# Kernel tuning notes

Measured on AMD Instinct MI355X. Metric: run time of the kernel, lower is better.

## Reference

```python
import jax, jax.numpy as jnp
import numpy as np

N_NODES = 4096
N_EDGES = 262144
D = 128
N_REL = 1000
N_ENT = 50000


def setup_inputs() -> dict:
    key = jax.random.key(0)
    ks = jax.random.split(key, 6)
    x = jax.random.normal(ks[0], (N_NODES, D), dtype=jnp.float32)
    edge_index = jax.random.randint(ks[1], (2, N_EDGES), 0, N_NODES)
    relation_id = jax.random.randint(ks[2], (N_EDGES,), 0, N_REL)
    neg_flag = jax.random.randint(ks[3], (N_EDGES,), 0, 2)
    rel_emb = jax.random.normal(ks[4], (N_REL, D), dtype=jnp.float32)
    entity_emb = jax.random.normal(ks[5], (N_ENT, D), dtype=jnp.float32)
    scale = jnp.ones((N_ENT,), dtype=jnp.float32)
    bias = jnp.zeros((N_ENT,), dtype=jnp.float32)
    return {"x": x, "edge_index": edge_index, "relation_id": relation_id,
            "neg_flag": neg_flag, "rel_emb": rel_emb, "entity_emb": entity_emb,
            "scale": scale, "bias": bias}


def reference(x, edge_index, relation_id, neg_flag, rel_emb, entity_emb, scale, bias):
    src, dst = edge_index[0], edge_index[1]
    # message: gather x_j, TransE tail estimate, sign flip for negated atoms
    neg_coef = 1.0 - 2.0 * neg_flag.astype(x.dtype)           # [E]
    msg = (x[src] + rel_emb[relation_id]) * neg_coef[:, None]  # [E, D]
    # aggregate: scatter-add into target nodes
    aggr_out = jax.ops.segment_sum(msg, dst, num_segments=x.shape[0])  # [N, D]
    # update: residual + bias/scale double-matmul through entity table
    aggr = 0.1 * x + aggr_out                                  # [N, D]
    entity_score = aggr @ entity_emb.T                          # [N, V]
    entity_score = jax.nn.relu(entity_score * scale + bias)
    out = entity_score @ entity_emb                             # [N, D]
    return out
```

## Files before the change

kernel.cpp:

```cpp
#include <hip/hip_runtime.h>
#include <stdint.h>

typedef __attribute__((ext_vector_type(8))) short short8;
typedef __attribute__((ext_vector_type(8))) unsigned short ushort8;
typedef __attribute__((ext_vector_type(4))) float f32x4;
typedef __attribute__((ext_vector_type(16))) float f32x16;
typedef __attribute__((ext_vector_type(2))) unsigned int uint2v;

#define NNODES 4096
#define NEDGES 262144
#define DIM 128
#define NENT 50000
#define NENTP 50048
#define PREPB 782
#define ETILE 32
#define NT32 1563
#define NSPLIT 24

__device__ __forceinline__ unsigned short f2bf(float f) {
  union { __bf16 b; unsigned short u; } c;
  c.b = (__bf16)f;
  return c.u;
}

__global__ __launch_bounds__(1024) void k_scan(
    const int* __restrict__ cnt, int* __restrict__ off, int* __restrict__ cur)
{
  __shared__ int s[1024];
  int t = threadIdx.x;
  int4 v = reinterpret_cast<const int4*>(cnt)[t];
  int lsum = v.x + v.y + v.z + v.w;
  s[t] = lsum; __syncthreads();
  for (int d = 1; d < 1024; d <<= 1) {
    int a = (t >= d) ? s[t - d] : 0;
    __syncthreads();
    s[t] += a;
    __syncthreads();
  }
  int base = s[t] - lsum;
  int4 o; o.x = base; o.y = base + v.x; o.z = o.y + v.y; o.w = o.z + v.z;
  reinterpret_cast<int4*>(off)[t] = o;
  reinterpret_cast<int4*>(cur)[t] = o;
  if (t == 1023) off[4096] = base + lsum;
}

__global__ __launch_bounds__(256) void k_place(
    const int* __restrict__ ei, const int* __restrict__ rid,
    const int* __restrict__ nf, int* __restrict__ cur, int* __restrict__ sorted)
{
  int e = blockIdx.x * 256 + threadIdx.x;
  int dst = ei[NEDGES + e];
  int pos = atomicAdd(&cur[dst], 1);
  sorted[pos] = ei[e] | (rid[e] << 12) | (nf[e] << 22);
}

__global__ __launch_bounds__(256) void k_aggr(
    const int* __restrict__ off, const int* __restrict__ sorted,
    const float* __restrict__ x, const float* __restrict__ rel,
    unsigned short* __restrict__ q)
{
  __shared__ float sAcc[8 * 132];
  const int n = blockIdx.x;
  const int t = threadIdx.x;
  const int slot = t >> 5;
  const int c = t & 31;
  const int b = off[n], eN = off[n + 1];
  float4 acc = make_float4(0.f, 0.f, 0.f, 0.f);
  for (int i = b + slot; i < eN; i += 8) {
    int p = sorted[i];
    float4 xv = reinterpret_cast<const float4*>(x)[(p & 4095) * 32 + c];
    float4 rv = reinterpret_cast<const float4*>(rel)[((p >> 12) & 1023) * 32 + c];
    float sgn = (p & (1 << 22)) ? -1.f : 1.f;
    acc.x += sgn * (xv.x + rv.x);
    acc.y += sgn * (xv.y + rv.y);
    acc.z += sgn * (xv.z + rv.z);
    acc.w += sgn * (xv.w + rv.w);
  }
  *reinterpret_cast<float4*>(&sAcc[slot * 132 + c * 4]) = acc;
  __syncthreads();
  if (t < 128) {
    float s = 0.f;
#pragma unroll
    for (int k = 0; k < 8; ++k) s += sAcc[k * 132 + t];
    q[n * DIM + t] = f2bf(0.1f * x[n * DIM + t] + s);
  }
}

__global__ __launch_bounds__(256) void k_prep(
    const float* __restrict__ ent, const float* __restrict__ scale,
    unsigned short* __restrict__ ebf, unsigned short* __restrict__ etbf,
    const int* __restrict__ ei, int* __restrict__ cnt)
{
  if (blockIdx.x >= PREPB) {
    int e = (blockIdx.x - PREPB) * 256 + threadIdx.x;
    atomicAdd(&cnt[ei[NEDGES + e]], 1);
    return;
  }
  __shared__ float sT[64 * 133];
  const int t = threadIdx.x;
  const int e0 = blockIdx.x * 64;
#pragma unroll
  for (int i = 0; i < 8; ++i) {
    int idx = i * 256 + t;
    int e = idx >> 5;
    int c4 = idx & 31;
    float4 v = make_float4(0.f, 0.f, 0.f, 0.f);
    float sc = 0.f;
    if (e0 + e < NENT) {
      v = reinterpret_cast<const float4*>(ent)[(e0 + e) * 32 + c4];
      sc = scale[e0 + e];
    }
    *reinterpret_cast<float4*>(&sT[e * 133 + c4 * 4]) = v;
    ushort4 bq;
    bq.x = f2bf(v.x * sc); bq.y = f2bf(v.y * sc);
    bq.z = f2bf(v.z * sc); bq.w = f2bf(v.w * sc);
    *reinterpret_cast<ushort4*>(&ebf[(e0 + e) * 128 + c4 * 4]) = bq;
  }
  __syncthreads();
  const int lane = t & 63;
  const int w = t >> 6;
  const int dl = lane >> 3;
  const int el = (lane & 7) * 8;
#pragma unroll
  for (int it = 0; it < 4; ++it) {
    int d = it * 32 + w * 8 + dl;
    ushort8 buf;
#pragma unroll
    for (int j = 0; j < 8; ++j) buf[j] = f2bf(sT[(el + j) * 133 + d]);
    *reinterpret_cast<ushort8*>(&etbf[d * NENTP + e0 + el]) = buf;
  }
}


__device__ __forceinline__ void gll16(const void* g, void* l) {
  __builtin_amdgcn_global_load_lds(
      (const __attribute__((address_space(1))) unsigned int*)g,
      (__attribute__((address_space(3))) unsigned int*)l, 16, 0, 0);
}

__device__ __forceinline__ unsigned cvtpk(float lo, float hi) {
  unsigned r;
  asm("v_cvt_pk_bf16_f32 %0, %1, %2" : "=v"(r) : "v"(lo), "v"(hi));
  return r;
}

__global__ __launch_bounds__(256, 3) void k_flash(
    const unsigned short* __restrict__ qg,
    const unsigned short* __restrict__ ebf,
    const unsigned short* __restrict__ etbf,
    const float* __restrict__ bias,
    float* __restrict__ out)
{
  __shared__ __align__(16) unsigned short sE[2][ETILE * 128];
  __shared__ __align__(16) unsigned short sET[2][128 * ETILE];
  __shared__ __align__(16) float sBias[2][ETILE];

  const int t = threadIdx.x;
  const int w = t >> 6;
  const int lane = t & 63;
  const int l31 = lane & 31;
  const int hi = lane >> 5;

  const int m0 = blockIdx.x * 128;
  const int tile_lo = (blockIdx.y * NT32) / NSPLIT;
  const int tile_hi = ((blockIdx.y + 1) * NT32) / NSPLIT;

  const int cE = (((t & 15) ^ ((t >> 4) & 15))) * 8;
  const int rE = t >> 4;
  const int cT = (((t & 3) ^ ((t >> 4) & 3))) * 8;
  const int rT = t >> 2;

  short8 qf[8];
  {
    const unsigned short* qrow = qg + (size_t)(m0 + w * 32 + l31) * DIM + hi * 8;
#pragma unroll
    for (int kk = 0; kk < 8; ++kk)
      qf[kk] = *reinterpret_cast<const short8*>(qrow + kk * 16);
  }

  f32x16 accO[4];
#pragma unroll
  for (int td = 0; td < 4; ++td)
#pragma unroll
    for (int r = 0; r < 16; ++r) accO[td][r] = 0.f;

  {
    const int vt = tile_lo * ETILE;
#pragma unroll
    for (int i = 0; i < 2; ++i)
      gll16(ebf + (size_t)(vt + i * 16 + rE) * DIM + cE, &sE[0][(i * 256 + t) * 8]);
#pragma unroll
    for (int i = 0; i < 2; ++i)
      gll16(etbf + (size_t)(i * 64 + rT) * NENTP + vt + cT, &sET[0][(i * 256 + t) * 8]);
    if (t < ETILE) sBias[0][t] = (vt + t < NENT) ? bias[vt + t] : 0.f;
  }
  __syncthreads();

  int cur = 0;
  for (int tile = tile_lo; tile < tile_hi; ++tile) {
    if (tile + 1 < tile_hi) {
      const int vt = (tile + 1) * ETILE;
#pragma unroll
      for (int i = 0; i < 2; ++i)
        gll16(ebf + (size_t)(vt + i * 16 + rE) * DIM + cE,
              &sE[cur ^ 1][(i * 256 + t) * 8]);
#pragma unroll
      for (int i = 0; i < 2; ++i)
        gll16(etbf + (size_t)(i * 64 + rT) * NENTP + vt + cT,
              &sET[cur ^ 1][(i * 256 + t) * 8]);
      if (t < ETILE) sBias[cur ^ 1][t] = (vt + t < NENT) ? bias[vt + t] : 0.f;
    }

    const unsigned short* sEc = sE[cur];
    const float* sb = sBias[cur];
    f32x16 accA, accB;
#pragma unroll
    for (int r = 0; r < 16; ++r) { accA[r] = 0.f; accB[r] = 0.f; }

    __builtin_amdgcn_s_setprio(1);
#pragma unroll
    for (int kk = 0; kk < 4; ++kk) {
      const int colA = ((kk * 4 + hi) ^ (l31 & 15)) * 8;
      const int colB = ((kk * 4 + 2 + hi) ^ (l31 & 15)) * 8;
      short8 a0 = *reinterpret_cast<const short8*>(&sEc[l31 * 128 + colA]);
      short8 a1 = *reinterpret_cast<const short8*>(&sEc[l31 * 128 + colB]);
      accA = __builtin_amdgcn_mfma_f32_32x32x16_bf16(a0, qf[2 * kk], accA, 0, 0, 0);
      accB = __builtin_amdgcn_mfma_f32_32x32x16_bf16(a1, qf[2 * kk + 1], accB, 0, 0, 0);
    }
    __builtin_amdgcn_s_setprio(0);

    short8 F[2];
    {
      float p[16];
#pragma unroll
      for (int g = 0; g < 4; ++g) {
        f32x4 b4 = *reinterpret_cast<const f32x4*>(&sb[g * 8 + hi * 4]);
#pragma unroll
        for (int j = 0; j < 4; ++j)
          p[g * 4 + j] = fmaxf(accA[g * 4 + j] + accB[g * 4 + j] + b4[j], 0.f);
      }
      unsigned wr[8];
#pragma unroll
      for (int c2 = 0; c2 < 8; ++c2) wr[c2] = cvtpk(p[2 * c2], p[2 * c2 + 1]);
      uint2v r02 = __builtin_amdgcn_permlane32_swap(wr[0], wr[2], false, false);
      uint2v r13 = __builtin_amdgcn_permlane32_swap(wr[1], wr[3], false, false);
      uint2v r46 = __builtin_amdgcn_permlane32_swap(wr[4], wr[6], false, false);
      uint2v r57 = __builtin_amdgcn_permlane32_swap(wr[5], wr[7], false, false);
      union { unsigned u[4]; short8 s; } f0, f1;
      f0.u[0] = r02[0]; f0.u[1] = r13[0]; f0.u[2] = r02[1]; f0.u[3] = r13[1];
      f1.u[0] = r46[0]; f1.u[1] = r57[0]; f1.u[2] = r46[1]; f1.u[3] = r57[1];
      F[0] = f0.s;
      F[1] = f1.s;
    }

    const unsigned short* sTc = sET[cur];
    const int keyT = (l31 >> 2) & 3;
    __builtin_amdgcn_s_setprio(1);
#pragma unroll
    for (int ke = 0; ke < 2; ++ke) {
      const int col = ((ke * 2 + hi) ^ keyT) * 8;
#pragma unroll
      for (int td = 0; td < 4; ++td) {
        const int d = td * 32 + l31;
        short8 bT = *reinterpret_cast<const short8*>(&sTc[d * ETILE + col]);
        accO[td] = __builtin_amdgcn_mfma_f32_32x32x16_bf16(F[ke], bT, accO[td], 0, 0, 0);
      }
    }
    __builtin_amdgcn_s_setprio(0);

    __syncthreads();
    cur ^= 1;
  }

#pragma unroll
  for (int td = 0; td < 4; ++td) {
#pragma unroll
    for (int r = 0; r < 16; ++r) {
      int qrow = (r & 3) + 8 * (r >> 2) + 4 * hi;
      int row = m0 + w * 32 + qrow;
      int col = td * 32 + l31;
      atomicAdd(&out[(size_t)row * DIM + col], accO[td][r]);
    }
  }
}

extern "C" void kernel_launch(void* const* d_in, const int* in_sizes, int n_in,
                              void* d_out, int out_size, void* d_ws, size_t ws_size,
                              hipStream_t stream) {
  const float* x     = (const float*)d_in[0];
  const int*   ei    = (const int*)d_in[1];
  const int*   rid   = (const int*)d_in[2];
  const int*   nf    = (const int*)d_in[3];
  const float* rel   = (const float*)d_in[4];
  const float* ent   = (const float*)d_in[5];
  const float* scale = (const float*)d_in[6];
  const float* bias  = (const float*)d_in[7];
  float* out = (float*)d_out;

  char* ws = (char*)d_ws;
  int*            cnt    = (int*)(ws + 0);
  int*            off    = (int*)(ws + (16u << 10));
  int*            cur    = (int*)(ws + (36u << 10));
  int*            sorted = (int*)(ws + (64u << 10));
  unsigned short* qb     = (unsigned short*)(ws + (1344u << 10));
  unsigned short* ebf    = (unsigned short*)(ws + (2560u << 10));
  unsigned short* etbf   = (unsigned short*)(ws + (2560u << 10) + (size_t)NENTP * DIM * 2);

  hipMemsetAsync(cnt, 0, 4096 * sizeof(int), stream);
  hipMemsetAsync(d_out, 0, (size_t)out_size * sizeof(float), stream);
  k_prep<<<PREPB + NEDGES / 256, 256, 0, stream>>>(ent, scale, ebf, etbf, ei, cnt);
  k_scan<<<1, 1024, 0, stream>>>(cnt, off, cur);
  k_place<<<NEDGES / 256, 256, 0, stream>>>(ei, rid, nf, cur, sorted);
  k_aggr<<<NNODES, 256, 0, stream>>>(off, sorted, x, rel, qb);
  k_flash<<<dim3(NNODES / 128, NSPLIT), 256, 0, stream>>>(qb, ebf, etbf, bias, out);
}
```

Baseline: 270.0 us.

## Software-pipeline score and output GEMMs with triple-buffered LDS tiles

Moves the entity-tile loop to a triple-buffered software pipeline. The score MFMAs for tile i+1 are issued alongside the output MFMAs for tile i, and loads run two tiles ahead. The aim is to hide the dependency stall between the score GEMM, the bias/ReLU/bf16 repack and the output GEMM, and to give global loads more lead time. LDS use per block grows by half, which could cut occupancy under the 3-blocks-per-CU launch bound.

```diff
diff --git a/kernel.cpp b/kernel.cpp
--- a/kernel.cpp
+++ b/kernel.cpp
@@ -151,9 +151,9 @@
     const float* __restrict__ bias,
     float* __restrict__ out)
 {
-  __shared__ __align__(16) unsigned short sE[2][ETILE * 128];
-  __shared__ __align__(16) unsigned short sET[2][128 * ETILE];
-  __shared__ __align__(16) float sBias[2][ETILE];
+  __shared__ __align__(16) unsigned short sE[3][ETILE * 128];
+  __shared__ __align__(16) unsigned short sET[3][128 * ETILE];
+  __shared__ __align__(16) float sBias[3][ETILE];
 
   const int t = threadIdx.x;
   const int w = t >> 6;
@@ -184,40 +184,22 @@
 #pragma unroll
     for (int r = 0; r < 16; ++r) accO[td][r] = 0.f;
 
-  {
-    const int vt = tile_lo * ETILE;
-#pragma unroll
-    for (int i = 0; i < 2; ++i)
-      gll16(ebf + (size_t)(vt + i * 16 + rE) * DIM + cE, &sE[0][(i * 256 + t) * 8]);
-#pragma unroll
-    for (int i = 0; i < 2; ++i)
-      gll16(etbf + (size_t)(i * 64 + rT) * NENTP + vt + cT, &sET[0][(i * 256 + t) * 8]);
-    if (t < ETILE) sBias[0][t] = (vt + t < NENT) ? bias[vt + t] : 0.f;
-  }
-  __syncthreads();
-
-  int cur = 0;
-  for (int tile = tile_lo; tile < tile_hi; ++tile) {
-    if (tile + 1 < tile_hi) {
-      const int vt = (tile + 1) * ETILE;
-#pragma unroll
-      for (int i = 0; i < 2; ++i)
-        gll16(ebf + (size_t)(vt + i * 16 + rE) * DIM + cE,
-              &sE[cur ^ 1][(i * 256 + t) * 8]);
-#pragma unroll
-      for (int i = 0; i < 2; ++i)
-        gll16(etbf + (size_t)(i * 64 + rT) * NENTP + vt + cT,
-              &sET[cur ^ 1][(i * 256 + t) * 8]);
-      if (t < ETILE) sBias[cur ^ 1][t] = (vt + t < NENT) ? bias[vt + t] : 0.f;
-    }
-
-    const unsigned short* sEc = sE[cur];
-    const float* sb = sBias[cur];
-    f32x16 accA, accB;
+  f32x16 accA, accB;
+  short8 F[2];
+
+  auto STAGE = [&](int tile, int buf) {
+    const int vt = tile * ETILE;
+    gll16(ebf + (size_t)(vt + rE) * DIM + cE, &sE[buf][t * 8]);
+    gll16(ebf + (size_t)(vt + 16 + rE) * DIM + cE, &sE[buf][(256 + t) * 8]);
+    gll16(etbf + (size_t)rT * NENTP + vt + cT, &sET[buf][t * 8]);
+    gll16(etbf + (size_t)(64 + rT) * NENTP + vt + cT, &sET[buf][(256 + t) * 8]);
+    if (t < ETILE) sBias[buf][t] = (vt + t < NENT) ? bias[vt + t] : 0.f;
+  };
+
+  auto SPHASE = [&](int buf) {
+    const unsigned short* sEc = sE[buf];
 #pragma unroll
     for (int r = 0; r < 16; ++r) { accA[r] = 0.f; accB[r] = 0.f; }
-
-    __builtin_amdgcn_s_setprio(1);
 #pragma unroll
     for (int kk = 0; kk < 4; ++kk) {
       const int colA = ((kk * 4 + hi) ^ (l31 & 15)) * 8;
@@ -227,35 +209,35 @@
       accA = __builtin_amdgcn_mfma_f32_32x32x16_bf16(a0, qf[2 * kk], accA, 0, 0, 0);
       accB = __builtin_amdgcn_mfma_f32_32x32x16_bf16(a1, qf[2 * kk + 1], accB, 0, 0, 0);
     }
-    __builtin_amdgcn_s_setprio(0);
-
-    short8 F[2];
-    {
-      float p[16];
-#pragma unroll
-      for (int g = 0; g < 4; ++g) {
-        f32x4 b4 = *reinterpret_cast<const f32x4*>(&sb[g * 8 + hi * 4]);
-#pragma unroll
-        for (int j = 0; j < 4; ++j)
-          p[g * 4 + j] = fmaxf(accA[g * 4 + j] + accB[g * 4 + j] + b4[j], 0.f);
-      }
-      unsigned wr[8];
-#pragma unroll
-      for (int c2 = 0; c2 < 8; ++c2) wr[c2] = cvtpk(p[2 * c2], p[2 * c2 + 1]);
-      uint2v r02 = __builtin_amdgcn_permlane32_swap(wr[0], wr[2], false, false);
-      uint2v r13 = __builtin_amdgcn_permlane32_swap(wr[1], wr[3], false, false);
-      uint2v r46 = __builtin_amdgcn_permlane32_swap(wr[4], wr[6], false, false);
-      uint2v r57 = __builtin_amdgcn_permlane32_swap(wr[5], wr[7], false, false);
-      union { unsigned u[4]; short8 s; } f0, f1;
-      f0.u[0] = r02[0]; f0.u[1] = r13[0]; f0.u[2] = r02[1]; f0.u[3] = r13[1];
-      f1.u[0] = r46[0]; f1.u[1] = r57[0]; f1.u[2] = r46[1]; f1.u[3] = r57[1];
-      F[0] = f0.s;
-      F[1] = f1.s;
-    }
-
-    const unsigned short* sTc = sET[cur];
+  };
+
+  auto REPACK = [&](int buf) {
+    const float* sb = sBias[buf];
+    float p[16];
+#pragma unroll
+    for (int g = 0; g < 4; ++g) {
+      f32x4 b4 = *reinterpret_cast<const f32x4*>(&sb[g * 8 + hi * 4]);
+#pragma unroll
+      for (int j = 0; j < 4; ++j)
+        p[g * 4 + j] = fmaxf(accA[g * 4 + j] + accB[g * 4 + j] + b4[j], 0.f);
+    }
+    unsigned wr[8];
+#pragma unroll
+    for (int c2 = 0; c2 < 8; ++c2) wr[c2] = cvtpk(p[2 * c2], p[2 * c2 + 1]);
+    uint2v r02 = __builtin_amdgcn_permlane32_swap(wr[0], wr[2], false, false);
+    uint2v r13 = __builtin_amdgcn_permlane32_swap(wr[1], wr[3], false, false);
+    uint2v r46 = __builtin_amdgcn_permlane32_swap(wr[4], wr[6], false, false);
+    uint2v r57 = __builtin_amdgcn_permlane32_swap(wr[5], wr[7], false, false);
+    union { unsigned u[4]; short8 s; } f0, f1;
+    f0.u[0] = r02[0]; f0.u[1] = r13[0]; f0.u[2] = r02[1]; f0.u[3] = r13[1];
+    f1.u[0] = r46[0]; f1.u[1] = r57[0]; f1.u[2] = r46[1]; f1.u[3] = r57[1];
+    F[0] = f0.s;
+    F[1] = f1.s;
+  };
+
+  auto OPHASE = [&](int buf) {
+    const unsigned short* sTc = sET[buf];
     const int keyT = (l31 >> 2) & 3;
-    __builtin_amdgcn_s_setprio(1);
 #pragma unroll
     for (int ke = 0; ke < 2; ++ke) {
       const int col = ((ke * 2 + hi) ^ keyT) * 8;
@@ -266,11 +248,31 @@
         accO[td] = __builtin_amdgcn_mfma_f32_32x32x16_bf16(F[ke], bT, accO[td], 0, 0, 0);
       }
     }
+  };
+
+  STAGE(tile_lo, 0);
+  if (tile_lo + 1 < tile_hi) STAGE(tile_lo + 1, 1);
+  __syncthreads();
+  SPHASE(0);
+
+  int cur = 0;
+  for (int tile = tile_lo; tile < tile_hi - 1; ++tile) {
+    int nx = cur + 1; if (nx == 3) nx = 0;
+    int st = nx + 1; if (st == 3) st = 0;
+    if (tile + 2 < tile_hi) STAGE(tile + 2, st);
+    REPACK(cur);
+    __builtin_amdgcn_s_setprio(1);
+    SPHASE(nx);
+    OPHASE(cur);
     __builtin_amdgcn_s_setprio(0);
-
     __syncthreads();
-    cur ^= 1;
-  }
+    cur = nx;
+  }
+
+  REPACK(cur);
+  __builtin_amdgcn_s_setprio(1);
+  OPHASE(cur);
+  __builtin_amdgcn_s_setprio(0);
 
 #pragma unroll
   for (int td = 0; td < 4; ++td) {
```

Measured after the change: 276.2 us. 2.3% more time.

## Fuse prep, scan, place and aggregate into one cooperative persistent kernel

Applied to the files above, without the earlier changes.

Merges the four preprocessing kernels (entity conversion plus degree count, prefix scan, edge placement, neighbor aggregation) into a single cooperative kernel of 768 persistent blocks separated by grid-wide syncs. The aim is to remove three kernel launch boundaries and their tail gaps. The scan now runs on one 256-thread block instead of 1024 threads. In exchange it adds grid.sync costs, leaves the machine idle during the single-block scan, and cuts the block count used by the aggregation loop.

```diff
diff --git a/kernel.cpp b/kernel.cpp
--- a/kernel.cpp
+++ b/kernel.cpp
@@ -1,5 +1,8 @@
 #include <hip/hip_runtime.h>
+#include <hip/hip_cooperative_groups.h>
 #include <stdint.h>
+
+namespace cg = cooperative_groups;
 
 typedef __attribute__((ext_vector_type(8))) short short8;
 typedef __attribute__((ext_vector_type(8))) unsigned short ushort8;
@@ -16,6 +19,7 @@
 #define ETILE 32
 #define NT32 1563
 #define NSPLIT 24
+#define NB 768
 
 __device__ __forceinline__ unsigned short f2bf(float f) {
   union { __bf16 b; unsigned short u; } c;
@@ -23,111 +27,124 @@
   return c.u;
 }
 
-__global__ __launch_bounds__(1024) void k_scan(
-    const int* __restrict__ cnt, int* __restrict__ off, int* __restrict__ cur)
+__global__ __launch_bounds__(256, 4) void k_pre(
+    const float* __restrict__ ent, const float* __restrict__ scale,
+    unsigned short* __restrict__ ebf, unsigned short* __restrict__ etbf,
+    const int* __restrict__ ei, const int* __restrict__ rid,
+    const int* __restrict__ nf, int* __restrict__ cnt,
+    int* __restrict__ off, int* __restrict__ cur, int* __restrict__ sorted,
+    const float* __restrict__ x, const float* __restrict__ rel,
+    unsigned short* __restrict__ qb)
 {
-  __shared__ int s[1024];
-  int t = threadIdx.x;
-  int4 v = reinterpret_cast<const int4*>(cnt)[t];
-  int lsum = v.x + v.y + v.z + v.w;
-  s[t] = lsum; __syncthreads();
-  for (int d = 1; d < 1024; d <<= 1) {
-    int a = (t >= d) ? s[t - d] : 0;
-    __syncthreads();
-    s[t] += a;
-    __syncthreads();
-  }
-  int base = s[t] - lsum;
-  int4 o; o.x = base; o.y = base + v.x; o.z = o.y + v.y; o.w = o.z + v.z;
-  reinterpret_cast<int4*>(off)[t] = o;
-  reinterpret_cast<int4*>(cur)[t] = o;
-  if (t == 1023) off[4096] = base + lsum;
-}
-
-__global__ __launch_bounds__(256) void k_place(
-    const int* __restrict__ ei, const int* __restrict__ rid,
-    const int* __restrict__ nf, int* __restrict__ cur, int* __restrict__ sorted)
-{
-  int e = blockIdx.x * 256 + threadIdx.x;
-  int dst = ei[NEDGES + e];
-  int pos = atomicAdd(&cur[dst], 1);
-  sorted[pos] = ei[e] | (rid[e] << 12) | (nf[e] << 22);
-}
-
-__global__ __launch_bounds__(256) void k_aggr(
-    const int* __restrict__ off, const int* __restrict__ sorted,
-    const float* __restrict__ x, const float* __restrict__ rel,
-    unsigned short* __restrict__ q)
-{
-  __shared__ float sAcc[8 * 132];
-  const int n = blockIdx.x;
+  cg::grid_group grid = cg::this_grid();
+  __shared__ __align__(16) char smem[64 * 133 * 4];
+  float* sT   = (float*)smem;
+  int*   sInt = (int*)smem;
+  float* sAcc = (float*)smem;
+
   const int t = threadIdx.x;
+  const int b = blockIdx.x;
+
+  for (int e = b * 256 + t; e < NEDGES; e += NB * 256)
+    atomicAdd(&cnt[ei[NEDGES + e]], 1);
+
+  for (int tile = b; tile < PREPB; tile += NB) {
+    const int e0 = tile * 64;
+#pragma unroll
+    for (int i = 0; i < 8; ++i) {
+      int idx = i * 256 + t;
+      int e = idx >> 5;
+      int c4 = idx & 31;
+      float4 v = make_float4(0.f, 0.f, 0.f, 0.f);
+      float sc = 0.f;
+      if (e0 + e < NENT) {
+        v = reinterpret_cast<const float4*>(ent)[(e0 + e) * 32 + c4];
+        sc = scale[e0 + e];
+      }
+      *reinterpret_cast<float4*>(&sT[e * 133 + c4 * 4]) = v;
+      ushort4 bq;
+      bq.x = f2bf(v.x * sc); bq.y = f2bf(v.y * sc);
+      bq.z = f2bf(v.z * sc); bq.w = f2bf(v.w * sc);
+      *reinterpret_cast<ushort4*>(&ebf[(e0 + e) * 128 + c4 * 4]) = bq;
+    }
+    __syncthreads();
+    const int lane = t & 63;
+    const int w = t >> 6;
+    const int dl = lane >> 3;
+    const int el = (lane & 7) * 8;
+#pragma unroll
+    for (int it = 0; it < 4; ++it) {
+      int d = it * 32 + w * 8 + dl;
+      ushort8 buf;
+#pragma unroll
+      for (int j = 0; j < 8; ++j) buf[j] = f2bf(sT[(el + j) * 133 + d]);
+      *reinterpret_cast<ushort8*>(&etbf[d * NENTP + e0 + el]) = buf;
+    }
+    __syncthreads();
+  }
+
+  grid.sync();
+
+  if (b == 0) {
+    int4 v[4];
+    int lsum = 0;
+#pragma unroll
+    for (int j = 0; j < 4; ++j) {
+      v[j] = reinterpret_cast<const int4*>(cnt)[t * 4 + j];
+      lsum += v[j].x + v[j].y + v[j].z + v[j].w;
+    }
+    sInt[t] = lsum; __syncthreads();
+    for (int d = 1; d < 256; d <<= 1) {
+      int a = (t >= d) ? sInt[t - d] : 0;
+      __syncthreads();
+      sInt[t] += a;
+      __syncthreads();
+    }
+    int base = sInt[t] - lsum;
+#pragma unroll
+    for (int j = 0; j < 4; ++j) {
+      int4 o; o.x = base; o.y = base + v[j].x; o.z = o.y + v[j].y; o.w = o.z + v[j].z;
+      base = o.w + v[j].w;
+      reinterpret_cast<int4*>(off)[t * 4 + j] = o;
+      reinterpret_cast<int4*>(cur)[t * 4 + j] = o;
+    }
+    if (t == 255) off[4096] = base;
+  }
+
+  grid.sync();
+
+  for (int e = b * 256 + t; e < NEDGES; e += NB * 256) {
+    int dst = ei[NEDGES + e];
+    int pos = atomicAdd(&cur[dst], 1);
+    sorted[pos] = ei[e] | (rid[e] << 12) | (nf[e] << 22);
+  }
+
+  grid.sync();
+
   const int slot = t >> 5;
   const int c = t & 31;
-  const int b = off[n], eN = off[n + 1];
-  float4 acc = make_float4(0.f, 0.f, 0.f, 0.f);
-  for (int i = b + slot; i < eN; i += 8) {
-    int p = sorted[i];
-    float4 xv = reinterpret_cast<const float4*>(x)[(p & 4095) * 32 + c];
-    float4 rv = reinterpret_cast<const float4*>(rel)[((p >> 12) & 1023) * 32 + c];
-    float sgn = (p & (1 << 22)) ? -1.f : 1.f;
-    acc.x += sgn * (xv.x + rv.x);
-    acc.y += sgn * (xv.y + rv.y);
-    acc.z += sgn * (xv.z + rv.z);
-    acc.w += sgn * (xv.w + rv.w);
-  }
-  *reinterpret_cast<float4*>(&sAcc[slot * 132 + c * 4]) = acc;
-  __syncthreads();
-  if (t < 128) {
-    float s = 0.f;
-#pragma unroll
-    for (int k = 0; k < 8; ++k) s += sAcc[k * 132 + t];
-    q[n * DIM + t] = f2bf(0.1f * x[n * DIM + t] + s);
-  }
-}
-
-__global__ __launch_bounds__(256) void k_prep(
-    const float* __restrict__ ent, const float* __restrict__ scale,
-    unsigned short* __restrict__ ebf, unsigned short* __restrict__ etbf,
-    const int* __restrict__ ei, int* __restrict__ cnt)
-{
-  if (blockIdx.x >= PREPB) {
-    int e = (blockIdx.x - PREPB) * 256 + threadIdx.x;
-    atomicAdd(&cnt[ei[NEDGES + e]], 1);
-    return;
-  }
-  __shared__ float sT[64 * 133];
-  const int t = threadIdx.x;
-  const int e0 = blockIdx.x * 64;
-#pragma unroll
-  for (int i = 0; i < 8; ++i) {
-    int idx = i * 256 + t;
-    int e = idx >> 5;
-    int c4 = idx & 31;
-    float4 v = make_float4(0.f, 0.f, 0.f, 0.f);
-    float sc = 0.f;
-    if (e0 + e < NENT) {
-      v = reinterpret_cast<const float4*>(ent)[(e0 + e) * 32 + c4];
-      sc = scale[e0 + e];
-    }
-    *reinterpret_cast<float4*>(&sT[e * 133 + c4 * 4]) = v;
-    ushort4 bq;
-    bq.x = f2bf(v.x * sc); bq.y = f2bf(v.y * sc);
-    bq.z = f2bf(v.z * sc); bq.w = f2bf(v.w * sc);
-    *reinterpret_cast<ushort4*>(&ebf[(e0 + e) * 128 + c4 * 4]) = bq;
-  }
-  __syncthreads();
-  const int lane = t & 63;
-  const int w = t >> 6;
-  const int dl = lane >> 3;
-  const int el = (lane & 7) * 8;
-#pragma unroll
-  for (int it = 0; it < 4; ++it) {
-    int d = it * 32 + w * 8 + dl;
-    ushort8 buf;
-#pragma unroll
-    for (int j = 0; j < 8; ++j) buf[j] = f2bf(sT[(el + j) * 133 + d]);
-    *reinterpret_cast<ushort8*>(&etbf[d * NENTP + e0 + el]) = buf;
+  for (int n = b; n < NNODES; n += NB) {
+    const int e0 = off[n], eN = off[n + 1];
+    float4 acc = make_float4(0.f, 0.f, 0.f, 0.f);
+    for (int i = e0 + slot; i < eN; i += 8) {
+      int p = sorted[i];
+      float4 xv = reinterpret_cast<const float4*>(x)[(p & 4095) * 32 + c];
+      float4 rv = reinterpret_cast<const float4*>(rel)[((p >> 12) & 1023) * 32 + c];
+      float sgn = (p & (1 << 22)) ? -1.f : 1.f;
+      acc.x += sgn * (xv.x + rv.x);
+      acc.y += sgn * (xv.y + rv.y);
+      acc.z += sgn * (xv.z + rv.z);
+      acc.w += sgn * (xv.w + rv.w);
+    }
+    *reinterpret_cast<float4*>(&sAcc[slot * 132 + c * 4]) = acc;
+    __syncthreads();
+    if (t < 128) {
+      float s = 0.f;
+#pragma unroll
+      for (int k = 0; k < 8; ++k) s += sAcc[k * 132 + t];
+      qb[n * DIM + t] = f2bf(0.1f * x[n * DIM + t] + s);
+    }
+    __syncthreads();
   }
 }
 
@@ -308,9 +325,15 @@
 
   hipMemsetAsync(cnt, 0, 4096 * sizeof(int), stream);
   hipMemsetAsync(d_out, 0, (size_t)out_size * sizeof(float), stream);
-  k_prep<<<PREPB + NEDGES / 256, 256, 0, stream>>>(ent, scale, ebf, etbf, ei, cnt);
-  k_scan<<<1, 1024, 0, stream>>>(cnt, off, cur);
-  k_place<<<NEDGES / 256, 256, 0, stream>>>(ei, rid, nf, cur, sorted);
-  k_aggr<<<NNODES, 256, 0, stream>>>(off, sorted, x, rel, qb);
+
+  void* args[] = {
+    (void*)&ent, (void*)&scale, (void*)&ebf, (void*)&etbf,
+    (void*)&ei, (void*)&rid, (void*)&nf, (void*)&cnt,
+    (void*)&off, (void*)&cur, (void*)&sorted,
+    (void*)&x, (void*)&rel, (void*)&qb
+  };
+  hipLaunchCooperativeKernel((const void*)k_pre, dim3(NB), dim3(256),
+                             args, 0, stream);
+
   k_flash<<<dim3(NNODES / 128, NSPLIT), 256, 0, stream>>>(qb, ebf, etbf, bias, out);
 }
```

New measurement: 553.0 us. 105% more time.
